# Kernel optimization log

Measured on AMD Instinct MI355X. Metric: run time of the kernel, lower is better.

The kernel has to match this reference:

```python
import jax, jax.numpy as jnp
import numpy as np

B, S, D, H, HD, RN, FF, WIN = 2, 2048, 2048, 16, 128, 32, 4096, 256
NEG = float(np.finfo(np.float16).min)  # torch.finfo(torch.float16).min
EPS = 1e-5
SCALE = 1.0 / float(np.sqrt(HD))


def _ln(x, w, b):
    m = jnp.mean(x, -1, keepdims=True)
    v = jnp.mean((x - m) ** 2, -1, keepdims=True)
    return (x - m) * jax.lax.rsqrt(v + EPS) * w + b


def _rms(x, w):
    return x * jax.lax.rsqrt(jnp.mean(x * x, -1, keepdims=True) + EPS) * w


def _rope_half(x, fc):
    # x: (B,S,H,RN); fc: (S,RN//2,2). Half-split input pairs, interleaved output
    # (faithful to apply_rotary_emb mode='half' + flatten(3)).
    half = x.shape[-1] // 2
    x0, x1 = x[..., :half], x[..., half:]
    c = fc[None, :, None, :, 0]
    s = fc[None, :, None, :, 1]
    out = jnp.stack([x0 * c - x1 * s, x1 * c + x0 * s], -1)  # (B,S,H,half,2)
    return out.reshape(x.shape)


def setup_inputs() -> dict:
    key = jax.random.key(0)
    ks = jax.random.split(key, 8)
    w = lambda k, shape: 0.02 * jax.random.normal(k, shape, jnp.float32)
    x = jax.random.normal(ks[0], (B, S, D), jnp.float32)
    # real rotary table: angles t * 10000^(-2i/RN), stored as (cos, sin)
    inv = 1.0 / (10000.0 ** (np.arange(0, RN, 2) / RN))  # (RN//2,)
    ang = np.arange(S)[:, None] * inv[None, :]           # (S, RN//2)
    freqs_cis = jnp.asarray(np.stack([np.cos(ang), np.sin(ang)], -1), jnp.float32)
    # sliding-window causal mask, window = 256
    i = np.arange(S)
    m = (i[None, :] <= i[:, None]) & ((i[:, None] - i[None, :]) < WIN)
    mask = jnp.asarray(m)[None, None]  # (1,1,S,S) bool
    return {
        "x": x, "freqs_cis": freqs_cis, "mask": mask,
        "wqkv_w": w(ks[1], (D, 3 * D)), "wqkv_b": jnp.zeros((3 * D,), jnp.float32),
        "wo_w": w(ks[2], (D, D)), "wo_b": jnp.zeros((D,), jnp.float32),
        "qn_w": jnp.ones((HD,), jnp.float32), "kn_w": jnp.ones((HD,), jnp.float32),
        "attn_ln_w": jnp.ones((D,), jnp.float32), "attn_ln_b": jnp.zeros((D,), jnp.float32),
        "ffn_ln_w": jnp.ones((D,), jnp.float32), "ffn_ln_b": jnp.zeros((D,), jnp.float32),
        "w1_w": w(ks[3], (D, FF)), "w1_b": jnp.zeros((FF,), jnp.float32),
        "w2_w": w(ks[4], (FF, D)), "w2_b": jnp.zeros((D,), jnp.float32),
    }


def reference(x, freqs_cis, mask, wqkv_w, wqkv_b, wo_w, wo_b, qn_w, kn_w,
              attn_ln_w, attn_ln_b, ffn_ln_w, ffn_ln_b, w1_w, w1_b, w2_w, w2_b):
    bsz, seqlen, _ = x.shape
    nx = _ln(x, attn_ln_w, attn_ln_b)
    qkv = nx @ wqkv_w + wqkv_b                       # (B,S,3D)
    q, k, v = jnp.split(qkv, [D, 2 * D], axis=-1)
    q = q.reshape(bsz, seqlen, H, HD)
    k = k.reshape(bsz, seqlen, H, HD)
    v = v.reshape(bsz, seqlen, H, HD)
    # QK-RMSNorm
    q, k = _rms(q, qn_w), _rms(k, kn_w)
    # partial rotary (first RN dims)
    q = jnp.concatenate([_rope_half(q[..., :RN], freqs_cis), q[..., RN:]], -1)
    k = jnp.concatenate([_rope_half(k[..., :RN], freqs_cis), k[..., RN:]], -1)
    # attention with windowed mask
    logits = jnp.einsum("bqhd,bkhd->bhqk", q, k) * SCALE
    logits = jnp.where(mask, logits, NEG)
    probs = jax.nn.softmax(logits, axis=-1)
    y = jnp.einsum("bhqk,bkhd->bqhd", probs, v).reshape(bsz, seqlen, D)
    attn_out = y @ wo_w + wo_b
    h = x + attn_out
    # parallel residual: FFN reads ffn_norm(res) with res = x
    f = _ln(x, ffn_ln_w, ffn_ln_b)
    ffn = jax.nn.gelu(f @ w1_w + w1_b, approximate=False) @ w2_w + w2_b
    return h + ffn
```

## Files before the change

kernel.cpp:

```cpp
#include <hip/hip_runtime.h>


typedef unsigned short u16;
typedef unsigned int   u32;
typedef __bf16 bf16x8 __attribute__((ext_vector_type(8)));
typedef float  f32x4  __attribute__((ext_vector_type(4)));
typedef __attribute__((address_space(3))) u32 as3_u32;
typedef __attribute__((address_space(1))) u32 as1_u32;

#define B_    2
#define S_    2048
#define D_    2048
#define H_    16
#define HD_   128
#define FF_   4096
#define WIN_  256
#define EPS_  1e-5f
#define SCALE_ 0.08838834764831845f

__device__ __forceinline__ float b2f(u16 u) {
    return __uint_as_float(((u32)u) << 16);
}
__device__ __forceinline__ u16 f2b(float f) {
    u32 u = __float_as_uint(f);
    u32 r = (u + 0x7fffu + ((u >> 16) & 1u)) >> 16;
    return (u16)r;
}
__device__ __forceinline__ float wave_sum(float v) {
#pragma unroll
    for (int o = 32; o > 0; o >>= 1) v += __shfl_xor(v, o);
    return v;
}
__device__ __forceinline__ void gld_lds16(const u16* g, u16* l) {
    __builtin_amdgcn_global_load_lds((const as1_u32*)g, (as3_u32*)l, 16, 0, 0);
}

__global__ __launch_bounds__(256) void transpose_k(const float* __restrict__ in,
                                                   u16* __restrict__ out,
                                                   int R, int C) {
    __shared__ float tile[64][65];
    int t = threadIdx.x;
    int r0 = blockIdx.y * 64, c0 = blockIdx.x * 64;
    int rr = t >> 2;
    int cb = (t & 3) * 16;
    const float* src = &in[(size_t)(r0 + rr) * C + c0 + cb];
#pragma unroll
    for (int j = 0; j < 16; j += 4) {
        float4 v = *(const float4*)&src[j];
        tile[rr][cb + j]     = v.x; tile[rr][cb + j + 1] = v.y;
        tile[rr][cb + j + 2] = v.z; tile[rr][cb + j + 3] = v.w;
    }
    __syncthreads();
    int wq = t & 31;
    int ch = t >> 5;
#pragma unroll
    for (int i = 0; i < 8; ++i) {
        int c = ch * 8 + i;
        u32 lo = (u32)f2b(tile[2 * wq][c]);
        u32 hi = (u32)f2b(tile[2 * wq + 1][c]);
        ((u32*)out)[(((size_t)(c0 + c) * R) >> 1) + (r0 >> 1) + wq] = lo | (hi << 16);
    }
}

__global__ __launch_bounds__(256) void ln_dual(const float* __restrict__ x,
        const float* __restrict__ aw, const float* __restrict__ ab,
        const float* __restrict__ fw, const float* __restrict__ fb,
        u16* __restrict__ nx, u16* __restrict__ f) {
    int row = blockIdx.x;
    const float* xr = x + (size_t)row * D_;
    int base = threadIdx.x * 8;
    float4 xa = *(const float4*)&xr[base];
    float4 xb = *(const float4*)&xr[base + 4];
    float xv[8] = {xa.x, xa.y, xa.z, xa.w, xb.x, xb.y, xb.z, xb.w};
    float s = 0.f, s2 = 0.f;
#pragma unroll
    for (int i = 0; i < 8; ++i) { s += xv[i]; s2 += xv[i] * xv[i]; }
    s = wave_sum(s); s2 = wave_sum(s2);
    __shared__ float r1[4], r2[4];
    int w = threadIdx.x >> 6;
    if ((threadIdx.x & 63) == 0) { r1[w] = s; r2[w] = s2; }
    __syncthreads();
    float ts  = r1[0] + r1[1] + r1[2] + r1[3];
    float ts2 = r2[0] + r2[1] + r2[2] + r2[3];
    float mean = ts * (1.f / D_);
    float var  = ts2 * (1.f / D_) - mean * mean;
    float inv  = rsqrtf(var + EPS_);
    float4 wa0 = *(const float4*)&aw[base], wa1 = *(const float4*)&aw[base + 4];
    float4 ba0 = *(const float4*)&ab[base], ba1 = *(const float4*)&ab[base + 4];
    float4 wf0 = *(const float4*)&fw[base], wf1 = *(const float4*)&fw[base + 4];
    float4 bf0 = *(const float4*)&fb[base], bf1 = *(const float4*)&fb[base + 4];
    float wav[8] = {wa0.x, wa0.y, wa0.z, wa0.w, wa1.x, wa1.y, wa1.z, wa1.w};
    float bav[8] = {ba0.x, ba0.y, ba0.z, ba0.w, ba1.x, ba1.y, ba1.z, ba1.w};
    float wfv[8] = {wf0.x, wf0.y, wf0.z, wf0.w, wf1.x, wf1.y, wf1.z, wf1.w};
    float bfv[8] = {bf0.x, bf0.y, bf0.z, bf0.w, bf1.x, bf1.y, bf1.z, bf1.w};
    union { uint4 v; u16 s[8]; } o1, o2;
#pragma unroll
    for (int i = 0; i < 8; ++i) {
        float t = (xv[i] - mean) * inv;
        o1.s[i] = f2b(t * wav[i] + bav[i]);
        o2.s[i] = f2b(t * wfv[i] + bfv[i]);
    }
    *(uint4*)&nx[(size_t)row * D_ + base] = o1.v;
    *(uint4*)&f [(size_t)row * D_ + base] = o2.v;
}

template <int EPI>
__global__ __launch_bounds__(256, 2) void gemm_bt(
        const u16* __restrict__ A, const u16* __restrict__ BT,
        const float* __restrict__ bias, const float* __restrict__ res,
        void* __restrict__ Cv, int M, int N, int K) {
    __shared__ __align__(16) u16 As[128][32];
    __shared__ __align__(16) u16 Bs[128][32];
    int m0 = blockIdx.y * 128, n0 = blockIdx.x * 128;
    int w = threadIdx.x >> 6, lane = threadIdx.x & 63;
    int wm = (w >> 1) * 64, wn = (w & 1) * 64;
    int row16 = lane & 15, quad = lane >> 4;
    int lr = lane >> 2;
    int lc = (lane & 3) * 8;
    f32x4 acc[4][4] = {};
    for (int k0 = 0; k0 < K; k0 += 32) {
        __syncthreads();
        gld_lds16(&A [(size_t)(m0 +      w * 16 + lr) * K + k0 + lc], &As[     w * 16][0]);
        gld_lds16(&A [(size_t)(m0 + 64 + w * 16 + lr) * K + k0 + lc], &As[64 + w * 16][0]);
        gld_lds16(&BT[(size_t)(n0 +      w * 16 + lr) * K + k0 + lc], &Bs[     w * 16][0]);
        gld_lds16(&BT[(size_t)(n0 + 64 + w * 16 + lr) * K + k0 + lc], &Bs[64 + w * 16][0]);
        __syncthreads();
        bf16x8 af[4], bfr[4];
#pragma unroll
        for (int i = 0; i < 4; ++i) {
            af[i]  = *(const bf16x8*)&As[wm + i * 16 + row16][quad * 8];
            bfr[i] = *(const bf16x8*)&Bs[wn + i * 16 + row16][quad * 8];
        }
#pragma unroll
        for (int mi = 0; mi < 4; ++mi)
#pragma unroll
            for (int ni = 0; ni < 4; ++ni)
                acc[mi][ni] = __builtin_amdgcn_mfma_f32_16x16x32_bf16(
                        af[mi], bfr[ni], acc[mi][ni], 0, 0, 0);
    }
#pragma unroll
    for (int mi = 0; mi < 4; ++mi) {
#pragma unroll
        for (int ni = 0; ni < 4; ++ni) {
            int gcol = n0 + wn + ni * 16 + row16;
            float bv = bias[gcol];
#pragma unroll
            for (int i = 0; i < 4; ++i) {
                int grow = m0 + wm + mi * 16 + quad * 4 + i;
                float vv = acc[mi][ni][i] + bv;
                if (EPI == 1) {
                    vv += res[(size_t)grow * N + gcol];
                    ((float*)Cv)[(size_t)grow * N + gcol] = vv;
                } else {
                    if (EPI == 2)
                        vv = vv * 0.5f * (1.0f + erff(vv * 0.70710678118654752f));
                    ((u16*)Cv)[(size_t)grow * N + gcol] = f2b(vv);
                }
            }
        }
    }
}

__global__ __launch_bounds__(256) void qk_rope(const u32* __restrict__ qkv32,
        const float* __restrict__ qn_w, const float* __restrict__ kn_w,
        const float* __restrict__ freqs,
        u32* __restrict__ q32, u32* __restrict__ k32) {
    int w = threadIdx.x >> 6, lane = threadIdx.x & 63;
    int unit = blockIdx.x * 4 + w;
    int h = unit & (H_ - 1);
    int s = (unit >> 4) & (S_ - 1);
    int b = unit >> 15;
    size_t inbase  = (size_t)(b * S_ + s) * (3 * D_ / 2) + h * (HD_ / 2);
    size_t outbase = ((size_t)((b * H_ + h) * S_) + s) * (HD_ / 2);
    float fc = 0.f, fs = 0.f;
    if (lane < 16) {
        fc = freqs[(s * 16 + lane) * 2];
        fs = freqs[(s * 16 + lane) * 2 + 1];
    }
#pragma unroll
    for (int part = 0; part < 2; ++part) {
        const float* nw = part ? kn_w : qn_w;
        u32 wv = qkv32[inbase + part * (D_ / 2) + lane];
        float a0 = b2f((u16)(wv & 0xffffu));
        float a1 = b2f((u16)(wv >> 16));
        float ss = wave_sum(a0 * a0 + a1 * a1);
        float inv = rsqrtf(ss * (1.f / HD_) + EPS_);
        float2 nwp = *(const float2*)&nw[2 * lane];
        float n0 = a0 * inv * nwp.x;
        float n1 = a1 * inv * nwp.y;
        float e0 = __shfl(n0, lane >> 1), e1 = __shfl(n1, lane >> 1);
        float o0 = __shfl(n0, 8 + (lane >> 1)), o1 = __shfl(n1, 8 + (lane >> 1));
        float x0 = (lane & 1) ? e1 : e0;
        float x1 = (lane & 1) ? o1 : o0;
        float rv0 = x0 * fc - x1 * fs;
        float rv1 = x1 * fc + x0 * fs;
        float w0 = (lane < 16) ? rv0 : n0;
        float w1 = (lane < 16) ? rv1 : n1;
        u32* dst = part ? k32 : q32;
        dst[outbase + lane] = (u32)f2b(w0) | ((u32)f2b(w1) << 16);
    }
}

__global__ __launch_bounds__(256) void v_transpose(const u32* __restrict__ qkv32,
                                                   u32* __restrict__ vt32) {
    __shared__ u32 tile[64][17];
    int bh = blockIdx.z; int b = bh >> 4, h = bh & 15;
    int s0 = blockIdx.x * 64, d0 = blockIdx.y * 32;
    int tid = threadIdx.x;
    int rr = tid >> 4, cc = tid & 15;
#pragma unroll
    for (int i = 0; i < 4; ++i) {
        int s = s0 + rr + i * 16;
        tile[rr + i * 16][cc] =
            qkv32[(size_t)(b * S_ + s) * (3 * D_ / 2) + (2 * D_ + h * HD_ + d0) / 2 + cc];
    }
    __syncthreads();
    int dr = tid & 31, sc = tid >> 5;
#pragma unroll
    for (int i = 0; i < 4; ++i) {
        int s2 = sc + i * 8;
        u32 w0 = tile[2 * s2][dr >> 1];
        u32 w1 = tile[2 * s2 + 1][dr >> 1];
        u32 h0 = (dr & 1) ? (w0 >> 16) : (w0 & 0xffffu);
        u32 h1 = (dr & 1) ? (w1 >> 16) : (w1 & 0xffffu);
        vt32[((size_t)bh * HD_ + d0 + dr) * (S_ / 2) + (s0 >> 1) + s2] = h0 | (h1 << 16);
    }
}

__global__ __launch_bounds__(256) void attn_mfma(
        const u16* __restrict__ q, const u16* __restrict__ k,
        const u16* __restrict__ vt, u16* __restrict__ y) {
    __shared__ __align__(16) u16 Ks [64][136];
    __shared__ __align__(16) u16 Vts[128][72];
    __shared__ __align__(16) u16 Ps [4][16][72];
    int g  = blockIdx.x & (S_ / 64 - 1);
    int bh = blockIdx.x >> 5;
    int qbase = g * 64;
    size_t kvbase = (size_t)bh * S_ * HD_;
    size_t vtbase = (size_t)bh * HD_ * S_;
    int w = threadIdx.x >> 6, lane = threadIdx.x & 63;
    int col16 = lane & 15, quad = lane >> 4;
    int q0w = qbase + w * 16;
    bf16x8 af[4];
#pragma unroll
    for (int kb = 0; kb < 4; ++kb)
        af[kb] = *(const bf16x8*)&q[kvbase + (size_t)(q0w + col16) * HD_ + kb * 32 + quad * 8];
    f32x4 oacc[8] = {};
    float mrow[4], lrow[4];
#pragma unroll
    for (int i = 0; i < 4; ++i) { mrow[i] = -1e38f; lrow[i] = 0.f; }
    int t0 = g >= 4 ? g - 4 : 0;
    int tid = threadIdx.x;
    int kr = tid >> 2, kc = (tid & 3) * 32;
    int vr = tid >> 1, vc = (tid & 1) * 32;
    for (int t = t0; t <= g; ++t) {
        __syncthreads();
        {
            const u16* kg = &k[kvbase + (size_t)(t * 64 + kr) * HD_ + kc];
#pragma unroll
            for (int i = 0; i < 4; ++i)
                *(uint4*)&Ks[kr][kc + i * 8] = *(const uint4*)&kg[i * 8];
            const u16* vg = &vt[vtbase + (size_t)vr * S_ + t * 64 + vc];
#pragma unroll
            for (int i = 0; i < 4; ++i)
                *(uint4*)&Vts[vr][vc + i * 8] = *(const uint4*)&vg[i * 8];
        }
        __syncthreads();
        f32x4 sacc[4] = {};
#pragma unroll
        for (int ks = 0; ks < 4; ++ks)
#pragma unroll
            for (int kb = 0; kb < 4; ++kb) {
                bf16x8 bf = *(const bf16x8*)&Ks[ks * 16 + col16][kb * 32 + quad * 8];
                sacc[ks] = __builtin_amdgcn_mfma_f32_16x16x32_bf16(af[kb], bf, sacc[ks], 0, 0, 0);
            }
        float pm[4][4];
        float tmax[4] = {-3e38f, -3e38f, -3e38f, -3e38f};
#pragma unroll
        for (int ks = 0; ks < 4; ++ks) {
            int jg = t * 64 + ks * 16 + col16;
#pragma unroll
            for (int i = 0; i < 4; ++i) {
                int qi = q0w + quad * 4 + i;
                bool valid = (jg <= qi) && (qi - jg < WIN_);
                float sv = valid ? sacc[ks][i] * SCALE_ : -3e38f;
                pm[ks][i] = sv;
                tmax[i] = fmaxf(tmax[i], sv);
            }
        }
#pragma unroll
        for (int off = 8; off >= 1; off >>= 1)
#pragma unroll
            for (int i = 0; i < 4; ++i)
                tmax[i] = fmaxf(tmax[i], __shfl_xor(tmax[i], off));
        float alpha[4], psum[4];
#pragma unroll
        for (int i = 0; i < 4; ++i) {
            float mnew = fmaxf(mrow[i], tmax[i]);
            alpha[i] = __expf(mrow[i] - mnew);
            mrow[i] = mnew;
            psum[i] = 0.f;
        }
#pragma unroll
        for (int ks = 0; ks < 4; ++ks)
#pragma unroll
            for (int i = 0; i < 4; ++i) {
                float p = __expf(pm[ks][i] - mrow[i]);
                psum[i] += p;
                Ps[w][quad * 4 + i][ks * 16 + col16] = f2b(p);
            }
#pragma unroll
        for (int off = 8; off >= 1; off >>= 1)
#pragma unroll
            for (int i = 0; i < 4; ++i)
                psum[i] += __shfl_xor(psum[i], off);
#pragma unroll
        for (int i = 0; i < 4; ++i)
            lrow[i] = lrow[i] * alpha[i] + psum[i];
#pragma unroll
        for (int ns = 0; ns < 8; ++ns)
#pragma unroll
            for (int i = 0; i < 4; ++i)
                oacc[ns][i] *= alpha[i];
#pragma unroll
        for (int c = 0; c < 2; ++c) {
            bf16x8 pf = *(const bf16x8*)&Ps[w][col16][c * 32 + quad * 8];
#pragma unroll
            for (int ns = 0; ns < 8; ++ns) {
                bf16x8 vf = *(const bf16x8*)&Vts[ns * 16 + col16][c * 32 + quad * 8];
                oacc[ns] = __builtin_amdgcn_mfma_f32_16x16x32_bf16(pf, vf, oacc[ns], 0, 0, 0);
            }
        }
    }
    int b = bh >> 4, hh = bh & 15;
#pragma unroll
    for (int i = 0; i < 4; ++i) {
        int qi = q0w + quad * 4 + i;
        float invl = 1.f / lrow[i];
        size_t ob = (size_t)(b * S_ + qi) * D_ + hh * HD_;
#pragma unroll
        for (int ns = 0; ns < 8; ++ns)
            y[ob + ns * 16 + col16] = f2b(oacc[ns][i] * invl);
    }
}

extern "C" void kernel_launch(void* const* d_in, const int* in_sizes, int n_in,
                              void* d_out, int out_size, void* d_ws, size_t ws_size,
                              hipStream_t stream) {
    const float* x      = (const float*)d_in[0];
    const float* freqs  = (const float*)d_in[1];
    const float* wqkv_w = (const float*)d_in[3];
    const float* wqkv_b = (const float*)d_in[4];
    const float* wo_w   = (const float*)d_in[5];
    const float* wo_b   = (const float*)d_in[6];
    const float* qn_w   = (const float*)d_in[7];
    const float* kn_w   = (const float*)d_in[8];
    const float* aln_w  = (const float*)d_in[9];
    const float* aln_b  = (const float*)d_in[10];
    const float* fln_w  = (const float*)d_in[11];
    const float* fln_b  = (const float*)d_in[12];
    const float* w1_w   = (const float*)d_in[13];
    const float* w1_b   = (const float*)d_in[14];
    const float* w2_w   = (const float*)d_in[15];
    const float* w2_b   = (const float*)d_in[16];
    float* out = (float*)d_out;

    char* ws = (char*)d_ws;
    size_t off = 0;
    auto alloc = [&](size_t bytes) { char* p = ws + off; off += (bytes + 255) & ~(size_t)255; return (u16*)p; };
    const size_t E = sizeof(u16);
    u16* wt_qkv = alloc((size_t)D_ * 3 * D_ * E);
    u16* wt_wo  = alloc((size_t)D_ * D_ * E);
    u16* wt_w1  = alloc((size_t)D_ * FF_ * E);
    u16* wt_w2  = alloc((size_t)FF_ * D_ * E);
    u16* nx     = alloc((size_t)B_ * S_ * D_ * E);
    u16* f      = alloc((size_t)B_ * S_ * D_ * E);
    u16* qkv    = alloc((size_t)B_ * S_ * 3 * D_ * E);
    u16* qb     = alloc((size_t)B_ * S_ * D_ * E);
    u16* kb     = alloc((size_t)B_ * S_ * D_ * E);
    u16* vtb    = alloc((size_t)B_ * S_ * D_ * E);
    u16* y    = nx;
    u16* tmid = qkv;
    float* h  = out;

    if (off > ws_size) return;

    const int M = B_ * S_;

    transpose_k<<<dim3(3 * D_ / 64, D_ / 64), 256, 0, stream>>>(wqkv_w, wt_qkv, D_, 3 * D_);
    transpose_k<<<dim3(D_ / 64, D_ / 64),     256, 0, stream>>>(wo_w,   wt_wo,  D_, D_);
    transpose_k<<<dim3(FF_ / 64, D_ / 64),    256, 0, stream>>>(w1_w,   wt_w1,  D_, FF_);
    transpose_k<<<dim3(D_ / 64, FF_ / 64),    256, 0, stream>>>(w2_w,   wt_w2,  FF_, D_);

    ln_dual<<<M, 256, 0, stream>>>(x, aln_w, aln_b, fln_w, fln_b, nx, f);

    gemm_bt<0><<<dim3(3 * D_ / 128, M / 128), 256, 0, stream>>>(nx, wt_qkv, wqkv_b, nullptr, qkv, M, 3 * D_, D_);

    qk_rope<<<B_ * S_ * H_ / 4, 256, 0, stream>>>((const u32*)qkv, qn_w, kn_w, freqs, (u32*)qb, (u32*)kb);
    v_transpose<<<dim3(S_ / 64, HD_ / 32, B_ * H_), 256, 0, stream>>>((const u32*)qkv, (u32*)vtb);

    attn_mfma<<<B_ * H_ * (S_ / 64), 256, 0, stream>>>(qb, kb, vtb, y);

    gemm_bt<2><<<dim3(FF_ / 128, M / 128), 256, 0, stream>>>(f, wt_w1, w1_b, nullptr, tmid, M, FF_, D_);

    gemm_bt<1><<<dim3(D_ / 128, M / 128), 256, 0, stream>>>(y, wt_wo, wo_b, x, h, M, D_, D_);

    gemm_bt<1><<<dim3(D_ / 128, M / 128), 256, 0, stream>>>(tmid, wt_w2, w2_b, h, out, M, D_, FF_);
}
```

Before: 688.3 us.

## Add 256x256-tile 8-wave pipelined GEMM for QKV and W1 projections

Adds a new GEMM kernel that uses 256x256 output tiles, 512 threads, double-buffered LDS filled with direct global-to-LDS loads, and a phased schedule that interleaves staging of future K tiles with MFMA work using explicit waitcnt and barriers. It also remaps workgroup IDs so tiles are spread across XCD groups, and raises MFMA issue priority. The QKV and W1 GEMMs switch to it, which raises arithmetic intensity per tile and overlaps loads with compute. The cost is large register and LDS use (128KB LDS, 2 blocks per CU requested) and fragile hand-written vmcnt accounting.

```diff
diff --git a/kernel.cpp b/kernel.cpp
--- a/kernel.cpp
+++ b/kernel.cpp
@@ -34,6 +34,14 @@
 __device__ __forceinline__ void gld_lds16(const u16* g, u16* l) {
     __builtin_amdgcn_global_load_lds((const as1_u32*)g, (as3_u32*)l, 16, 0, 0);
 }
+__device__ __forceinline__ void block_bar() {
+    asm volatile("" ::: "memory");
+    __builtin_amdgcn_s_barrier();
+    asm volatile("" ::: "memory");
+}
+#define VMCNT4()  asm volatile("s_waitcnt vmcnt(4)" ::: "memory")
+#define VMCNT0()  asm volatile("s_waitcnt vmcnt(0)" ::: "memory")
+#define LGKMCNT0() asm volatile("s_waitcnt lgkmcnt(0)" ::: "memory")
 
 __global__ __launch_bounds__(256) void transpose_k(const float* __restrict__ in,
                                                    u16* __restrict__ out,
@@ -161,6 +169,140 @@
     }
 }
 
+template <int EPI>
+__global__ __launch_bounds__(512, 2) void gemm256_bt(
+        const u16* __restrict__ A, const u16* __restrict__ BT,
+        const float* __restrict__ bias, const float* __restrict__ res,
+        void* __restrict__ Cv, int M, int N, int K, int nbx) {
+    __shared__ __align__(16) u16 sm[2][2][256][64];
+    int nwg = gridDim.x;
+    int cpx = nwg >> 3;
+    int bid = blockIdx.x;
+    int sid = (bid & 7) * cpx + (bid >> 3);
+    int bx = sid % nbx, by = sid / nbx;
+    int m0 = by * 256, n0 = bx * 256;
+
+    int w = threadIdx.x >> 6, lane = threadIdx.x & 63;
+    int wm = (w >> 2) * 128, wn = (w & 3) * 64;
+    int row16 = lane & 15, quad = lane >> 4;
+    int xr = (lane & 7) << 3;
+    int lr = lane >> 3;
+    int lcs = ((lane & 7) ^ lr) << 3;
+
+    auto stage = [&](int bb, int mat, int hh, int t) {
+        const u16* src = mat ? BT : A;
+        int r0 = (mat ? n0 : m0) + hh * 128;
+        int cc = t * 64 + lcs;
+#pragma unroll
+        for (int j = 0; j < 2; ++j) {
+            int rb = (w * 2 + j) * 8;
+            gld_lds16(&src[(size_t)(r0 + rb + lr) * K + cc],
+                      &sm[bb][mat][hh * 128 + rb][0]);
+        }
+    };
+
+    f32x4 acc[8][4] = {};
+    bf16x8 af[4][2];
+    bf16x8 bq[2][2][2];
+
+    int nt = K >> 6;
+    int niter = nt >> 1;
+
+    stage(0, 0, 0, 0); stage(0, 1, 0, 0); stage(0, 1, 1, 0); stage(0, 0, 1, 0);
+    stage(1, 1, 0, 1); stage(1, 1, 1, 1);
+    VMCNT4();
+    block_bar();
+
+    for (int i = 0; i < niter; ++i) {
+        bool last = (i == niter - 1);
+        int tb = 2 * i + 1, tc = 2 * i + 2, td = 2 * i + 3;
+#pragma unroll
+        for (int ph = 0; ph < 8; ++ph) {
+            const int bb = ph >> 2;
+            const int h  = ph & 3;
+            const int mh = h >> 1, nh = h & 1;
+            if (h == 0) {
+#pragma unroll
+                for (int m2 = 0; m2 < 4; ++m2)
+#pragma unroll
+                    for (int ks = 0; ks < 2; ++ks)
+                        af[m2][ks] = *(const bf16x8*)
+                            &sm[bb][0][wm + m2 * 16 + row16][(ks * 32 + quad * 8) ^ xr];
+#pragma unroll
+                for (int n2 = 0; n2 < 2; ++n2)
+#pragma unroll
+                    for (int ks = 0; ks < 2; ++ks)
+                        bq[0][n2][ks] = *(const bf16x8*)
+                            &sm[bb][1][wn + n2 * 16 + row16][(ks * 32 + quad * 8) ^ xr];
+            } else if (h == 1) {
+#pragma unroll
+                for (int n2 = 0; n2 < 2; ++n2)
+#pragma unroll
+                    for (int ks = 0; ks < 2; ++ks)
+                        bq[1][n2][ks] = *(const bf16x8*)
+                            &sm[bb][1][wn + 32 + n2 * 16 + row16][(ks * 32 + quad * 8) ^ xr];
+            } else if (h == 2) {
+#pragma unroll
+                for (int m2 = 0; m2 < 4; ++m2)
+#pragma unroll
+                    for (int ks = 0; ks < 2; ++ks)
+                        af[m2][ks] = *(const bf16x8*)
+                            &sm[bb][0][wm + 64 + m2 * 16 + row16][(ks * 32 + quad * 8) ^ xr];
+            }
+            if (ph == 0) stage(1, 0, 0, tb);
+            else if (ph == 1) stage(1, 0, 1, tb);
+            else if (!last) {
+                if      (ph == 2) stage(0, 1, 0, tc);
+                else if (ph == 3) stage(0, 1, 1, tc);
+                else if (ph == 4) stage(0, 0, 0, tc);
+                else if (ph == 5) stage(0, 0, 1, tc);
+                else if (ph == 6) stage(1, 1, 0, td);
+                else if (ph == 7) stage(1, 1, 1, td);
+            }
+            block_bar();
+            LGKMCNT0();
+            __builtin_amdgcn_s_setprio(1);
+#pragma unroll
+            for (int m2 = 0; m2 < 4; ++m2)
+#pragma unroll
+                for (int n2 = 0; n2 < 2; ++n2)
+#pragma unroll
+                    for (int ks = 0; ks < 2; ++ks)
+                        acc[mh * 4 + m2][nh * 2 + n2] =
+                            __builtin_amdgcn_mfma_f32_16x16x32_bf16(
+                                af[m2][ks], bq[nh][n2][ks],
+                                acc[mh * 4 + m2][nh * 2 + n2], 0, 0, 0);
+            __builtin_amdgcn_s_setprio(0);
+            if (h == 3) {
+                if (ph == 3 && last) { VMCNT0(); } else { VMCNT4(); }
+            }
+            block_bar();
+        }
+    }
+
+#pragma unroll
+    for (int mi = 0; mi < 8; ++mi) {
+#pragma unroll
+        for (int ni = 0; ni < 4; ++ni) {
+            int gcol = n0 + wn + ni * 16 + row16;
+            float bv = bias[gcol];
+#pragma unroll
+            for (int i2 = 0; i2 < 4; ++i2) {
+                int grow = m0 + wm + mi * 16 + quad * 4 + i2;
+                float vv = acc[mi][ni][i2] + bv;
+                if (EPI == 1) {
+                    vv += res[(size_t)grow * N + gcol];
+                    ((float*)Cv)[(size_t)grow * N + gcol] = vv;
+                } else {
+                    if (EPI == 2)
+                        vv = vv * 0.5f * (1.0f + erff(vv * 0.70710678118654752f));
+                    ((u16*)Cv)[(size_t)grow * N + gcol] = f2b(vv);
+                }
+            }
+        }
+    }
+}
+
 __global__ __launch_bounds__(256) void qk_rope(const u32* __restrict__ qkv32,
         const float* __restrict__ qn_w, const float* __restrict__ kn_w,
         const float* __restrict__ freqs,
@@ -394,14 +536,16 @@
 
     ln_dual<<<M, 256, 0, stream>>>(x, aln_w, aln_b, fln_w, fln_b, nx, f);
 
-    gemm_bt<0><<<dim3(3 * D_ / 128, M / 128), 256, 0, stream>>>(nx, wt_qkv, wqkv_b, nullptr, qkv, M, 3 * D_, D_);
+    gemm256_bt<0><<<(3 * D_ / 256) * (M / 256), 512, 0, stream>>>(
+            nx, wt_qkv, wqkv_b, nullptr, qkv, M, 3 * D_, D_, 3 * D_ / 256);
 
     qk_rope<<<B_ * S_ * H_ / 4, 256, 0, stream>>>((const u32*)qkv, qn_w, kn_w, freqs, (u32*)qb, (u32*)kb);
     v_transpose<<<dim3(S_ / 64, HD_ / 32, B_ * H_), 256, 0, stream>>>((const u32*)qkv, (u32*)vtb);
 
     attn_mfma<<<B_ * H_ * (S_ / 64), 256, 0, stream>>>(qb, kb, vtb, y);
 
-    gemm_bt<2><<<dim3(FF_ / 128, M / 128), 256, 0, stream>>>(f, wt_w1, w1_b, nullptr, tmid, M, FF_, D_);
+    gemm256_bt<2><<<(FF_ / 256) * (M / 256), 512, 0, stream>>>(
+            f, wt_w1, w1_b, nullptr, tmid, M, FF_, D_, FF_ / 256);
 
     gemm_bt<1><<<dim3(D_ / 128, M / 128), 256, 0, stream>>>(y, wt_wo, wo_b, x, h, M, D_, D_);
 
```

Result: slower. 860.8 us (+25.1%).

## Double GEMM K-tile to 64 with XOR-swizzled LDS and prefetch attention K/V tiles

Applied to the files above, without the earlier changes.

The GEMM main loop now stages 64-wide K tiles, which halves the number of barrier-separated iterations and doubles the MFMA work between syncs. The LDS columns are XOR-swizzled by row so fragment reads avoid bank conflicts. The attention kernel now loads the next K/V tile into registers while computing on the current tile, overlapping global latency with MFMA work. The cost is more LDS and registers, which may reduce occupancy.

```diff
diff --git a/kernel.cpp b/kernel.cpp
--- a/kernel.cpp
+++ b/kernel.cpp
@@ -109,34 +109,41 @@
         const u16* __restrict__ A, const u16* __restrict__ BT,
         const float* __restrict__ bias, const float* __restrict__ res,
         void* __restrict__ Cv, int M, int N, int K) {
-    __shared__ __align__(16) u16 As[128][32];
-    __shared__ __align__(16) u16 Bs[128][32];
+    __shared__ __align__(16) u16 As[128][64];
+    __shared__ __align__(16) u16 Bs[128][64];
     int m0 = blockIdx.y * 128, n0 = blockIdx.x * 128;
     int w = threadIdx.x >> 6, lane = threadIdx.x & 63;
     int wm = (w >> 1) * 64, wn = (w & 1) * 64;
     int row16 = lane & 15, quad = lane >> 4;
-    int lr = lane >> 2;
-    int lc = (lane & 3) * 8;
+    int lr  = lane >> 3;
+    int lcs = ((lane & 7) ^ lr) << 3;
+    int xr  = (lane & 7) << 3;
     f32x4 acc[4][4] = {};
-    for (int k0 = 0; k0 < K; k0 += 32) {
+    for (int k0 = 0; k0 < K; k0 += 64) {
         __syncthreads();
-        gld_lds16(&A [(size_t)(m0 +      w * 16 + lr) * K + k0 + lc], &As[     w * 16][0]);
-        gld_lds16(&A [(size_t)(m0 + 64 + w * 16 + lr) * K + k0 + lc], &As[64 + w * 16][0]);
-        gld_lds16(&BT[(size_t)(n0 +      w * 16 + lr) * K + k0 + lc], &Bs[     w * 16][0]);
-        gld_lds16(&BT[(size_t)(n0 + 64 + w * 16 + lr) * K + k0 + lc], &Bs[64 + w * 16][0]);
+#pragma unroll
+        for (int j = 0; j < 4; ++j) {
+            int rb = w * 32 + j * 8;
+            gld_lds16(&A [(size_t)(m0 + rb + lr) * K + k0 + lcs], &As[rb][0]);
+            gld_lds16(&BT[(size_t)(n0 + rb + lr) * K + k0 + lcs], &Bs[rb][0]);
+        }
         __syncthreads();
-        bf16x8 af[4], bfr[4];
-#pragma unroll
-        for (int i = 0; i < 4; ++i) {
-            af[i]  = *(const bf16x8*)&As[wm + i * 16 + row16][quad * 8];
-            bfr[i] = *(const bf16x8*)&Bs[wn + i * 16 + row16][quad * 8];
-        }
+        bf16x8 af[4][2], bfr[4][2];
+#pragma unroll
+        for (int i = 0; i < 4; ++i)
+#pragma unroll
+            for (int ks = 0; ks < 2; ++ks) {
+                af[i][ks]  = *(const bf16x8*)&As[wm + i * 16 + row16][(ks * 32 + quad * 8) ^ xr];
+                bfr[i][ks] = *(const bf16x8*)&Bs[wn + i * 16 + row16][(ks * 32 + quad * 8) ^ xr];
+            }
 #pragma unroll
         for (int mi = 0; mi < 4; ++mi)
 #pragma unroll
             for (int ni = 0; ni < 4; ++ni)
-                acc[mi][ni] = __builtin_amdgcn_mfma_f32_16x16x32_bf16(
-                        af[mi], bfr[ni], acc[mi][ni], 0, 0, 0);
+#pragma unroll
+                for (int ks = 0; ks < 2; ++ks)
+                    acc[mi][ni] = __builtin_amdgcn_mfma_f32_16x16x32_bf16(
+                            af[mi][ks], bfr[ni][ks], acc[mi][ni], 0, 0, 0);
     }
 #pragma unroll
     for (int mi = 0; mi < 4; ++mi) {
@@ -253,17 +260,33 @@
     int tid = threadIdx.x;
     int kr = tid >> 2, kc = (tid & 3) * 32;
     int vr = tid >> 1, vc = (tid & 1) * 32;
+    uint4 krA[4], vrA[4];
+    {
+        const u16* kg = &k[kvbase + (size_t)(t0 * 64 + kr) * HD_ + kc];
+        const u16* vg = &vt[vtbase + (size_t)vr * S_ + t0 * 64 + vc];
+#pragma unroll
+        for (int i = 0; i < 4; ++i) {
+            krA[i] = *(const uint4*)&kg[i * 8];
+            vrA[i] = *(const uint4*)&vg[i * 8];
+        }
+    }
     for (int t = t0; t <= g; ++t) {
         __syncthreads();
-        {
-            const u16* kg = &k[kvbase + (size_t)(t * 64 + kr) * HD_ + kc];
-#pragma unroll
-            for (int i = 0; i < 4; ++i)
-                *(uint4*)&Ks[kr][kc + i * 8] = *(const uint4*)&kg[i * 8];
-            const u16* vg = &vt[vtbase + (size_t)vr * S_ + t * 64 + vc];
-#pragma unroll
-            for (int i = 0; i < 4; ++i)
-                *(uint4*)&Vts[vr][vc + i * 8] = *(const uint4*)&vg[i * 8];
+#pragma unroll
+        for (int i = 0; i < 4; ++i) {
+            *(uint4*)&Ks[kr][kc + i * 8]  = krA[i];
+            *(uint4*)&Vts[vr][vc + i * 8] = vrA[i];
+        }
+        uint4 krB[4], vrB[4];
+        bool more = (t < g);
+        if (more) {
+            const u16* kg = &k[kvbase + (size_t)((t + 1) * 64 + kr) * HD_ + kc];
+            const u16* vg = &vt[vtbase + (size_t)vr * S_ + (t + 1) * 64 + vc];
+#pragma unroll
+            for (int i = 0; i < 4; ++i) {
+                krB[i] = *(const uint4*)&kg[i * 8];
+                vrB[i] = *(const uint4*)&vg[i * 8];
+            }
         }
         __syncthreads();
         f32x4 sacc[4] = {};
@@ -330,6 +353,10 @@
                 bf16x8 vf = *(const bf16x8*)&Vts[ns * 16 + col16][c * 32 + quad * 8];
                 oacc[ns] = __builtin_amdgcn_mfma_f32_16x16x32_bf16(pf, vf, oacc[ns], 0, 0, 0);
             }
+        }
+        if (more) {
+#pragma unroll
+            for (int i = 0; i < 4; ++i) { krA[i] = krB[i]; vrA[i] = vrB[i]; }
         }
     }
     int b = bh >> 4, hh = bh & 15;
```

After: 706.5 us. 2.6% more time.
